# Kernel tuning notes

Hardware: AMD Instinct MI355X
Metric: run time of the kernel (lower is better)

## Reference

```python
import jax, jax.numpy as jnp
import numpy as np

NUM_HEADS = 32
HEAD_DIM = 128
NUM_KV_HEADS = 8
SCALE = 0.08838834764831845  # 1/sqrt(128)
SEQ_LEN = 2048


def setup_inputs() -> dict:
    key = jax.random.key(0)
    kq, kk, kv = jax.random.split(key, 3)
    q = jax.random.normal(kq, (SEQ_LEN, NUM_HEADS * HEAD_DIM), dtype=jnp.float32)
    k = jax.random.normal(kk, (SEQ_LEN, NUM_KV_HEADS * HEAD_DIM), dtype=jnp.float32)
    v = jax.random.normal(kv, (SEQ_LEN, NUM_KV_HEADS * HEAD_DIM), dtype=jnp.float32)
    return {"q": q, "k": k, "v": v}


def reference(q, k, v):
    S = q.shape[0]
    qh = q.reshape(S, NUM_HEADS, HEAD_DIM)            # [S, H, D]
    kh = k.reshape(S, NUM_KV_HEADS, HEAD_DIM)         # [S, KVH, D]
    vh = v.reshape(S, NUM_KV_HEADS, HEAD_DIM)
    # GQA: repeat_interleave along head dim
    expand = NUM_HEADS // NUM_KV_HEADS
    kh = jnp.repeat(kh, expand, axis=1)               # [S, H, D]
    vh = jnp.repeat(vh, expand, axis=1)
    scores = jnp.einsum('ihd,jhd->ihj', qh, kh) * SCALE  # [S, H, S]
    causal = jnp.triu(jnp.ones((S, S), dtype=bool), k=1)  # True above diagonal
    scores = jnp.where(causal[:, None, :], jnp.float32(-jnp.inf), scores)
    weights = jax.nn.softmax(scores, axis=-1)
    o = jnp.einsum('ihj,jhd->ihd', weights, vh)       # [S, H, D]
    return o.reshape(S, NUM_HEADS * HEAD_DIM)
```

## Files before the change

kernel.cpp:

```cpp
#include <hip/hip_runtime.h>


#define SEQ   2048
#define NH    32
#define NKV   8
#define HD    128
#define QLD   4096
#define KLD   1024
#define KVB   32

typedef __attribute__((ext_vector_type(8))) __bf16 bf16x8;
typedef __attribute__((ext_vector_type(4))) __bf16 bf16x4;
typedef __attribute__((ext_vector_type(2))) __bf16 bf16x2;
typedef __attribute__((ext_vector_type(4))) float  f32x4;
typedef __attribute__((ext_vector_type(4))) short  s16x4;
typedef __attribute__((ext_vector_type(2))) unsigned int u32x2;

static __device__ __forceinline__ unsigned int pack2(float lo, float hi) {
  bf16x2 t; t[0] = (__bf16)lo; t[1] = (__bf16)hi;
  return __builtin_bit_cast(unsigned int, t);
}

static __device__ __forceinline__ f32x4 mfma16(bf16x4 a, u32x2 b, f32x4 c) {
#if __has_builtin(__builtin_amdgcn_mfma_f32_16x16x16bf16_1k)
  return __builtin_amdgcn_mfma_f32_16x16x16bf16_1k(
      __builtin_bit_cast(s16x4, a), __builtin_bit_cast(s16x4, b), c, 0, 0, 0);
#else
  asm volatile("v_mfma_f32_16x16x16_bf16 %0, %1, %2, %0"
               : "+v"(c) : "v"(a), "v"(b));
  return c;
#endif
}

__global__ void prep_tiles(const float* __restrict__ k, __bf16* __restrict__ kt,
                           const float* __restrict__ v, __bf16* __restrict__ vtt) {
  __shared__ __bf16 TT[HD][34];
  const int bx  = blockIdx.x;
  const int tid = threadIdx.x;
  const int kl  = tid >> 3;
  const int dc  = tid & 7;
  if (bx < 512) {
    const int kvh = bx >> 6, t = bx & 63;
    const float* src = k + (size_t)(t * 32 + kl) * KLD + kvh * HD + dc * 16;
    __bf16* dst = kt + (size_t)(kvh * 64 + t) * 4096;
    const int g = kl >> 4, l15 = kl & 15;
#pragma unroll
    for (int h = 0; h < 2; ++h) {
      const int d0 = dc * 16 + h * 8;
      const int c = d0 >> 5, quad = (d0 >> 3) & 3;
      float4 a0 = *(const float4*)(src + h * 8);
      float4 a1 = *(const float4*)(src + h * 8 + 4);
      bf16x8 f;
      f[0] = (__bf16)a0.x; f[1] = (__bf16)a0.y; f[2] = (__bf16)a0.z; f[3] = (__bf16)a0.w;
      f[4] = (__bf16)a1.x; f[5] = (__bf16)a1.y; f[6] = (__bf16)a1.z; f[7] = (__bf16)a1.w;
      const int slot = g * 256 + c * 64 + quad * 16 + l15;
      *(bf16x8*)(dst + slot * 8) = f;
    }
  } else {
    const int b = bx - 512, kvh = b >> 6, t = b & 63;
    const float* src = v + (size_t)(t * 32 + kl) * KLD + kvh * HD + dc * 16;
#pragma unroll
    for (int jj = 0; jj < 4; ++jj) {
      float4 x = *(const float4*)(src + jj * 4);
      const int d = dc * 16 + jj * 4;
      TT[d + 0][kl] = (__bf16)x.x; TT[d + 1][kl] = (__bf16)x.y;
      TT[d + 2][kl] = (__bf16)x.z; TT[d + 3][kl] = (__bf16)x.w;
    }
    __syncthreads();
    __bf16* dst = vtt + (size_t)(kvh * 64 + t) * 4096;
#pragma unroll
    for (int ss = 0; ss < 2; ++ss) {
      const int s   = tid + ss * 256;
      const int nt  = s >> 6, quad = (s >> 4) & 3, l15 = s & 15;
      const int dim = nt * 16 + l15;
      bf16x8 f;
#pragma unroll
      for (int e = 0; e < 4; ++e) {
        f[e]     = TT[dim][quad * 4 + e];
        f[4 + e] = TT[dim][16 + quad * 4 + e];
      }
      *(bf16x8*)(dst + s * 8) = f;
    }
  }
}

__global__ __launch_bounds__(256, 2)
void fa_kernel(const float* __restrict__ q, const __bf16* __restrict__ kt,
               const __bf16* __restrict__ vtt, float* __restrict__ out) {
  const int bid  = blockIdx.x;
  const int kvh  = bid & 7;
  const int slot = bid >> 3;
  const int head = kvh * 4 + (slot & 3);
  const int ip   = slot >> 2;
  const int tid  = threadIdx.x;
  const int wave = tid >> 6;
  const int lane = tid & 63;
  const int l15  = lane & 15;
  const int quad = lane >> 4;

  const int rwS[2] = { (31 - ip) * 64 + wave * 16, ip * 64 + wave * 16 };

  constexpr float QS = 0.08838834764831845f * 1.4426950408889634f;

  bf16x8 qf[2][4];
#pragma unroll
  for (int sub = 0; sub < 2; ++sub) {
    const float* qp = q + (size_t)(rwS[sub] + l15) * QLD + head * HD + quad * 8;
#pragma unroll
    for (int c = 0; c < 4; ++c) {
      float4 a0 = *(const float4*)(qp + c * 32);
      float4 a1 = *(const float4*)(qp + c * 32 + 4);
      bf16x8 f;
      f[0] = (__bf16)(a0.x * QS); f[1] = (__bf16)(a0.y * QS);
      f[2] = (__bf16)(a0.z * QS); f[3] = (__bf16)(a0.w * QS);
      f[4] = (__bf16)(a1.x * QS); f[5] = (__bf16)(a1.y * QS);
      f[6] = (__bf16)(a1.z * QS); f[7] = (__bf16)(a1.w * QS);
      qf[sub][c] = f;
    }
  }

  const __bf16* KT0 = kt  + (size_t)(kvh * 64) * 4096;
  const __bf16* VT0 = vtt + (size_t)(kvh * 64) * 4096;
  const int loff = lane * 8;

  f32x4 acc[2][8];
  f32x4 lp[2];
#pragma unroll
  for (int sub = 0; sub < 2; ++sub) {
    lp[sub] = (f32x4){0.f, 0.f, 0.f, 0.f};
#pragma unroll
    for (int nt = 0; nt < 8; ++nt) acc[sub][nt] = (f32x4){0.f, 0.f, 0.f, 0.f};
  }

  const int ntiles = 64 - 2 * ip;

  bf16x8 kk0[2][4], kk1[2][4];
#pragma unroll
  for (int g = 0; g < 2; ++g)
#pragma unroll
    for (int c = 0; c < 4; ++c)
      kk0[g][c] = *(const bf16x8*)(KT0 + g * 2048 + c * 512 + loff);

  auto body = [&](int t, bf16x8 (&kc)[2][4], bf16x8 (&kn)[2][4]) {
    bf16x8 vv[8];
    const __bf16* vtile = VT0 + (size_t)t * 4096;
#pragma unroll
    for (int nt = 0; nt < 8; ++nt)
      vv[nt] = *(const bf16x8*)(vtile + nt * 512 + loff);
    if (t + 1 < ntiles) {
      const __bf16* ktile = KT0 + (size_t)(t + 1) * 4096;
#pragma unroll
      for (int g = 0; g < 2; ++g)
#pragma unroll
        for (int c = 0; c < 4; ++c)
          kn[g][c] = *(const bf16x8*)(ktile + g * 2048 + c * 512 + loff);
    }

    const bool l_on = (t <= 2 * ip + 1);

    u32x2 pknew[2][2];
#pragma unroll
    for (int g = 0; g < 2; ++g) {
#pragma unroll
      for (int sub = 0; sub < 2; ++sub) {
        if (sub == 1 && !l_on) continue;
        f32x4 s = (f32x4){0.f, 0.f, 0.f, 0.f};
        __builtin_amdgcn_s_setprio(1);
#pragma unroll
        for (int c = 0; c < 4; ++c)
          s = __builtin_amdgcn_mfma_f32_16x16x32_bf16(kc[g][c], qf[sub][c], s, 0, 0, 0);
        __builtin_amdgcn_s_setprio(0);
        if (t * KVB + KVB - 1 > rwS[sub]) {
          const int key0  = t * KVB + g * 16 + quad * 4;
          const int myrow = rwS[sub] + l15;
#pragma unroll
          for (int e = 0; e < 4; ++e)
            if (key0 + e > myrow) s[e] = -1e30f;
        }
        f32x4 p;
#pragma unroll
        for (int e = 0; e < 4; ++e) p[e] = __builtin_amdgcn_exp2f(s[e]);
        lp[sub] += p;
        u32x2 pkk;
        pkk.x = pack2(p[0], p[1]);
        pkk.y = pack2(p[2], p[3]);
        pknew[sub][g] = pkk;
      }
    }

#pragma unroll
    for (int kt2 = 0; kt2 < 2; ++kt2) {
      __builtin_amdgcn_s_setprio(1);
#pragma unroll
      for (int nt = 0; nt < 8; ++nt) {
        bf16x4 vf;
#pragma unroll
        for (int e = 0; e < 4; ++e) vf[e] = vv[nt][kt2 * 4 + e];
        acc[0][nt] = mfma16(vf, pknew[0][kt2], acc[0][nt]);
        if (l_on)
          acc[1][nt] = mfma16(vf, pknew[1][kt2], acc[1][nt]);
      }
      __builtin_amdgcn_s_setprio(0);
    }

    __builtin_amdgcn_s_barrier();
  };

  for (int t = 0; t < ntiles; t += 2) {
    body(t,     kk0, kk1);
    body(t + 1, kk1, kk0);
  }

#pragma unroll
  for (int sub = 0; sub < 2; ++sub) {
    float ls = lp[sub][0] + lp[sub][1] + lp[sub][2] + lp[sub][3];
    ls += __shfl_xor(ls, 16);
    ls += __shfl_xor(ls, 32);
    const float inv = 1.0f / ls;
    float* op = out + (size_t)(rwS[sub] + l15) * QLD + head * HD + quad * 4;
#pragma unroll
    for (int nt = 0; nt < 8; ++nt) {
      f32x4 r = acc[sub][nt];
      float4 w = {r[0] * inv, r[1] * inv, r[2] * inv, r[3] * inv};
      *(float4*)(op + nt * 16) = w;
    }
  }
}

extern "C" void kernel_launch(void* const* d_in, const int* in_sizes, int n_in,
                              void* d_out, int out_size, void* d_ws, size_t ws_size,
                              hipStream_t stream) {
  const float* q = (const float*)d_in[0];
  const float* k = (const float*)d_in[1];
  const float* v = (const float*)d_in[2];
  float* o = (float*)d_out;
  __bf16* ktb = (__bf16*)d_ws;
  __bf16* vtb = (__bf16*)d_ws + (size_t)SEQ * KLD;
  prep_tiles<<<1024, 256, 0, stream>>>(k, ktb, v, vtb);
  fa_kernel<<<512, 256, 0, stream>>>(q, ktb, vtb, o);
}
```

Baseline: 154.4 us.

## Split KV range across two wave groups per block and merge via LDS

Doubles the block to 512 threads with two 4-wave groups. Each group processes half of the key tiles for a row tile, processing the high and low row tiles as two sequential phases instead of interleaving both. Partial accumulators and row sums from the second group are combined through shared memory before normalization and output. This is meant to raise wave-level parallelism and shorten the per-wave serial KV loop. In exchange it adds LDS traffic, extra block-wide syncs, duplicated Q loads, and halved register budget under the new launch bounds.

Measured after the change: 447.2 us. 190% more time.

```diff
diff --git a/kernel.cpp b/kernel.cpp
--- a/kernel.cpp
+++ b/kernel.cpp
@@ -84,95 +84,82 @@
   }
 }
 
-__global__ __launch_bounds__(256, 2)
+__global__ __launch_bounds__(512, 4)
 void fa_kernel(const float* __restrict__ q, const __bf16* __restrict__ kt,
                const __bf16* __restrict__ vtt, float* __restrict__ out) {
+  __shared__ float CAcc[4][2048];
+  __shared__ float CLp[4][256];
+
   const int bid  = blockIdx.x;
   const int kvh  = bid & 7;
   const int slot = bid >> 3;
   const int head = kvh * 4 + (slot & 3);
   const int ip   = slot >> 2;
   const int tid  = threadIdx.x;
-  const int wave = tid >> 6;
+  const int w    = tid >> 6;
+  const int wg   = w >> 2;
+  const int wl   = w & 3;
   const int lane = tid & 63;
   const int l15  = lane & 15;
   const int quad = lane >> 4;
 
-  const int rwS[2] = { (31 - ip) * 64 + wave * 16, ip * 64 + wave * 16 };
-
   constexpr float QS = 0.08838834764831845f * 1.4426950408889634f;
-
-  bf16x8 qf[2][4];
-#pragma unroll
-  for (int sub = 0; sub < 2; ++sub) {
-    const float* qp = q + (size_t)(rwS[sub] + l15) * QLD + head * HD + quad * 8;
-#pragma unroll
-    for (int c = 0; c < 4; ++c) {
-      float4 a0 = *(const float4*)(qp + c * 32);
-      float4 a1 = *(const float4*)(qp + c * 32 + 4);
-      bf16x8 f;
-      f[0] = (__bf16)(a0.x * QS); f[1] = (__bf16)(a0.y * QS);
-      f[2] = (__bf16)(a0.z * QS); f[3] = (__bf16)(a0.w * QS);
-      f[4] = (__bf16)(a1.x * QS); f[5] = (__bf16)(a1.y * QS);
-      f[6] = (__bf16)(a1.z * QS); f[7] = (__bf16)(a1.w * QS);
-      qf[sub][c] = f;
-    }
-  }
 
   const __bf16* KT0 = kt  + (size_t)(kvh * 64) * 4096;
   const __bf16* VT0 = vtt + (size_t)(kvh * 64) * 4096;
   const int loff = lane * 8;
 
-  f32x4 acc[2][8];
-  f32x4 lp[2];
-#pragma unroll
-  for (int sub = 0; sub < 2; ++sub) {
-    lp[sub] = (f32x4){0.f, 0.f, 0.f, 0.f};
-#pragma unroll
-    for (int nt = 0; nt < 8; ++nt) acc[sub][nt] = (f32x4){0.f, 0.f, 0.f, 0.f};
-  }
-
-  const int ntiles = 64 - 2 * ip;
-
-  bf16x8 kk0[2][4], kk1[2][4];
-#pragma unroll
-  for (int g = 0; g < 2; ++g)
-#pragma unroll
-    for (int c = 0; c < 4; ++c)
-      kk0[g][c] = *(const bf16x8*)(KT0 + g * 2048 + c * 512 + loff);
-
-  auto body = [&](int t, bf16x8 (&kc)[2][4], bf16x8 (&kn)[2][4]) {
-    bf16x8 vv[8];
-    const __bf16* vtile = VT0 + (size_t)t * 4096;
-#pragma unroll
-    for (int nt = 0; nt < 8; ++nt)
-      vv[nt] = *(const bf16x8*)(vtile + nt * 512 + loff);
-    if (t + 1 < ntiles) {
-      const __bf16* ktile = KT0 + (size_t)(t + 1) * 4096;
-#pragma unroll
-      for (int g = 0; g < 2; ++g)
-#pragma unroll
-        for (int c = 0; c < 4; ++c)
-          kn[g][c] = *(const bf16x8*)(ktile + g * 2048 + c * 512 + loff);
-    }
-
-    const bool l_on = (t <= 2 * ip + 1);
-
-    u32x2 pknew[2][2];
-#pragma unroll
-    for (int g = 0; g < 2; ++g) {
-#pragma unroll
-      for (int sub = 0; sub < 2; ++sub) {
-        if (sub == 1 && !l_on) continue;
+  auto phase = [&](int rowtile, int t0, int nkt) {
+    const int rowbase = rowtile * 64 + wl * 16;
+
+    bf16x8 qf[4];
+    {
+      const float* qp = q + (size_t)(rowbase + l15) * QLD + head * HD + quad * 8;
+#pragma unroll
+      for (int c = 0; c < 4; ++c) {
+        float4 a0 = *(const float4*)(qp + c * 32);
+        float4 a1 = *(const float4*)(qp + c * 32 + 4);
+        bf16x8 f;
+        f[0] = (__bf16)(a0.x * QS); f[1] = (__bf16)(a0.y * QS);
+        f[2] = (__bf16)(a0.z * QS); f[3] = (__bf16)(a0.w * QS);
+        f[4] = (__bf16)(a1.x * QS); f[5] = (__bf16)(a1.y * QS);
+        f[6] = (__bf16)(a1.z * QS); f[7] = (__bf16)(a1.w * QS);
+        qf[c] = f;
+      }
+    }
+
+    f32x4 acc[8];
+    f32x4 lp = (f32x4){0.f, 0.f, 0.f, 0.f};
+#pragma unroll
+    for (int nt = 0; nt < 8; ++nt) acc[nt] = (f32x4){0.f, 0.f, 0.f, 0.f};
+
+    bf16x8 kk0[2][4], kk1[2][4];
+#pragma unroll
+    for (int g = 0; g < 2; ++g)
+#pragma unroll
+      for (int c = 0; c < 4; ++c)
+        kk0[g][c] = *(const bf16x8*)(KT0 + (size_t)t0 * 4096 + g * 2048 + c * 512 + loff);
+
+    auto body = [&](int tt, bf16x8 (&kc)[2][4], bf16x8 (&kn)[2][4]) {
+      const int t = t0 + tt;
+      bf16x8 vv[8];
+      const __bf16* vtile = VT0 + (size_t)t * 4096;
+#pragma unroll
+      for (int nt = 0; nt < 8; ++nt)
+        vv[nt] = *(const bf16x8*)(vtile + nt * 512 + loff);
+
+      u32x2 pknew[2];
+#pragma unroll
+      for (int g = 0; g < 2; ++g) {
         f32x4 s = (f32x4){0.f, 0.f, 0.f, 0.f};
         __builtin_amdgcn_s_setprio(1);
 #pragma unroll
         for (int c = 0; c < 4; ++c)
-          s = __builtin_amdgcn_mfma_f32_16x16x32_bf16(kc[g][c], qf[sub][c], s, 0, 0, 0);
+          s = __builtin_amdgcn_mfma_f32_16x16x32_bf16(kc[g][c], qf[c], s, 0, 0, 0);
         __builtin_amdgcn_s_setprio(0);
-        if (t * KVB + KVB - 1 > rwS[sub]) {
+        if (t * KVB + KVB - 1 > rowbase) {
           const int key0  = t * KVB + g * 16 + quad * 4;
-          const int myrow = rwS[sub] + l15;
+          const int myrow = rowbase + l15;
 #pragma unroll
           for (int e = 0; e < 4; ++e)
             if (key0 + e > myrow) s[e] = -1e30f;
@@ -180,51 +167,74 @@
         f32x4 p;
 #pragma unroll
         for (int e = 0; e < 4; ++e) p[e] = __builtin_amdgcn_exp2f(s[e]);
-        lp[sub] += p;
+        lp += p;
         u32x2 pkk;
         pkk.x = pack2(p[0], p[1]);
         pkk.y = pack2(p[2], p[3]);
-        pknew[sub][g] = pkk;
-      }
-    }
-
-#pragma unroll
-    for (int kt2 = 0; kt2 < 2; ++kt2) {
-      __builtin_amdgcn_s_setprio(1);
+        pknew[g] = pkk;
+      }
+
+      if (tt + 1 < nkt) {
+        const __bf16* ktile = KT0 + (size_t)(t + 1) * 4096;
+#pragma unroll
+        for (int g = 0; g < 2; ++g)
+#pragma unroll
+          for (int c = 0; c < 4; ++c)
+            kn[g][c] = *(const bf16x8*)(ktile + g * 2048 + c * 512 + loff);
+      }
+
+#pragma unroll
+      for (int kt2 = 0; kt2 < 2; ++kt2) {
+        __builtin_amdgcn_s_setprio(1);
+#pragma unroll
+        for (int nt = 0; nt < 8; ++nt) {
+          bf16x4 vf;
+#pragma unroll
+          for (int e = 0; e < 4; ++e) vf[e] = vv[nt][kt2 * 4 + e];
+          acc[nt] = mfma16(vf, pknew[kt2], acc[nt]);
+        }
+        __builtin_amdgcn_s_setprio(0);
+      }
+      __builtin_amdgcn_s_barrier();
+    };
+
+    int tt = 0;
+    for (; tt + 2 <= nkt; tt += 2) {
+      body(tt,     kk0, kk1);
+      body(tt + 1, kk1, kk0);
+    }
+    if (tt < nkt) body(tt, kk0, kk1);
+
+    if (wg == 1) {
+#pragma unroll
+      for (int nt = 0; nt < 8; ++nt)
+        *(f32x4*)&CAcc[wl][nt * 256 + lane * 4] = acc[nt];
+      *(f32x4*)&CLp[wl][lane * 4] = lp;
+    }
+    __syncthreads();
+    if (wg == 0) {
+      f32x4 plp = *(const f32x4*)&CLp[wl][lane * 4];
+      lp += plp;
+      float ls = lp[0] + lp[1] + lp[2] + lp[3];
+      ls += __shfl_xor(ls, 16);
+      ls += __shfl_xor(ls, 32);
+      const float inv = 1.0f / ls;
+      float* op = out + (size_t)(rowbase + l15) * QLD + head * HD + quad * 4;
 #pragma unroll
       for (int nt = 0; nt < 8; ++nt) {
-        bf16x4 vf;
-#pragma unroll
-        for (int e = 0; e < 4; ++e) vf[e] = vv[nt][kt2 * 4 + e];
-        acc[0][nt] = mfma16(vf, pknew[0][kt2], acc[0][nt]);
-        if (l_on)
-          acc[1][nt] = mfma16(vf, pknew[1][kt2], acc[1][nt]);
-      }
-      __builtin_amdgcn_s_setprio(0);
-    }
-
-    __builtin_amdgcn_s_barrier();
+        f32x4 pa = *(const f32x4*)&CAcc[wl][nt * 256 + lane * 4];
+        f32x4 r = acc[nt] + pa;
+        float4 wv = {r[0] * inv, r[1] * inv, r[2] * inv, r[3] * inv};
+        *(float4*)(op + nt * 16) = wv;
+      }
+    }
+    __syncthreads();
   };
 
-  for (int t = 0; t < ntiles; t += 2) {
-    body(t,     kk0, kk1);
-    body(t + 1, kk1, kk0);
-  }
-
-#pragma unroll
-  for (int sub = 0; sub < 2; ++sub) {
-    float ls = lp[sub][0] + lp[sub][1] + lp[sub][2] + lp[sub][3];
-    ls += __shfl_xor(ls, 16);
-    ls += __shfl_xor(ls, 32);
-    const float inv = 1.0f / ls;
-    float* op = out + (size_t)(rwS[sub] + l15) * QLD + head * HD + quad * 4;
-#pragma unroll
-    for (int nt = 0; nt < 8; ++nt) {
-      f32x4 r = acc[sub][nt];
-      float4 w = {r[0] * inv, r[1] * inv, r[2] * inv, r[3] * inv};
-      *(float4*)(op + nt * 16) = w;
-    }
-  }
+  const int nH = 32 - ip;
+  phase(31 - ip, wg * nH, nH);
+  const int nL = ip + 1;
+  phase(ip, wg * nL, nL);
 }
 
 extern "C" void kernel_launch(void* const* d_in, const int* in_sizes, int n_in,
@@ -237,5 +247,5 @@
   __bf16* ktb = (__bf16*)d_ws;
   __bf16* vtb = (__bf16*)d_ws + (size_t)SEQ * KLD;
   prep_tiles<<<1024, 256, 0, stream>>>(k, ktb, v, vtb);
-  fa_kernel<<<512, 256, 0, stream>>>(q, ktb, vtb, o);
-}
+  fa_kernel<<<512, 512, 0, stream>>>(q, ktb, vtb, o);
+}
```
